# Kernel optimization log

Hardware: AMD Instinct MI355X
Metric: run time of the kernel (lower is better)

Reference implementation:

```python
import jax, jax.numpy as jnp
import numpy as np

N = 8192      # number of WSI patches
DIN = 1024    # input patch-feature dim (dim_in)
DH = 256      # dim_hidden
K = 6         # topk
SCALE = DH ** -0.5

def leaky(x):
    return jax.nn.leaky_relu(x, 0.01)

def setup_inputs() -> dict:
    key = jax.random.key(0)
    ks = jax.random.split(key, 8)
    def w(k, shape, fan_in):
        return jax.random.normal(k, shape, jnp.float32) / np.sqrt(fan_in).astype(np.float32)
    return {
        "x_path": jax.random.normal(ks[0], (N, DIN), jnp.float32),
        "fc1_W": w(ks[1], (DIN, DH), DIN), "fc1_b": jnp.zeros((DH,), jnp.float32),
        "Wh": w(ks[2], (DH, DH), DH), "bh": jnp.zeros((DH,), jnp.float32),
        "Wt": w(ks[3], (DH, DH), DH), "bt": jnp.zeros((DH,), jnp.float32),
        "W1": w(ks[4], (DH, DH), DH), "b1": jnp.zeros((DH,), jnp.float32),
        "W2": w(ks[5], (DH, DH), DH), "b2": jnp.zeros((DH,), jnp.float32),
        "Ag1": w(ks[6], (DH, DH // 2), DH), "bg1": jnp.zeros((DH // 2,), jnp.float32),
        "Ag2": w(ks[7], (DH // 2, 1), DH // 2), "bg2": jnp.zeros((1,), jnp.float32),
    }

def reference(x_path, fc1_W, fc1_b, Wh, bh, Wt, bt, W1, b1, W2, b2, Ag1, bg1, Ag2, bg2):
    # _fc1: Linear(1024->256) + LeakyReLU, then add global mean ("*0.5" mixing)
    x = leaky(x_path @ fc1_W + fc1_b)[None]                 # (1,N,DH)
    x = (x + x.mean(axis=1, keepdims=True)) * 0.5
    e_h = x @ Wh + bh                                        # (1,N,DH)
    e_t = x @ Wt + bt                                        # (1,N,DH)
    # dense attention logits, then top-k neighbor selection
    attn_logit = (e_h * SCALE) @ jnp.swapaxes(e_t, -1, -2)   # (1,N,N)
    topk_w, topk_i = jax.lax.top_k(attn_logit, K)            # (1,N,K)
    p = jax.nn.softmax(topk_w, axis=2)                       # (1,N,K)
    Nb_h = e_t[0][topk_i[0]][None]                           # gather: (1,N,K,DH)
    # message construction
    eh_r = p[..., None] * Nb_h + (1.0 - p)[..., None] * e_h[:, :, None, :]
    gate = jnp.tanh(e_h[:, :, None, :] + eh_r)               # (1,N,K,DH)
    # faithful to torch.einsum('ijkl,ijkm->ijk', Nb_h, gate):
    # l and m are independent -> separable double sum
    ka_w = Nb_h.sum(-1) * gate.sum(-1)                       # (1,N,K)
    ka_p = jax.nn.softmax(ka_w, axis=2)
    e_Nh = jnp.einsum('ink,inkd->ind', ka_p, Nb_h)           # (1,N,DH)
    # message MLPs (dropout in eval mode = identity)
    e_msg = leaky((e_h + e_Nh) @ W1 + b1) + leaky((e_h * e_Nh) @ W2 + b2)
    # GlobalAttention readout: gate_nn = Linear(256,128)+LeakyReLU+Linear(128,1)
    x2 = e_msg[0]                                            # (N,DH)
    g = leaky(x2 @ Ag1 + bg1) @ Ag2 + bg2                    # (N,1)
    g = jax.nn.softmax(g, axis=0)
    e_g = (g * x2).sum(axis=0, keepdims=True)                # (1,DH)
    return e_msg, e_g
```

## Files before the change

kernel.cpp:

```cpp
#include <hip/hip_runtime.h>


typedef __attribute__((ext_vector_type(8))) short short8;
typedef __attribute__((ext_vector_type(4))) short short4v;
typedef __attribute__((ext_vector_type(4))) float f32x4;

__device__ inline float bf2f(unsigned short b) {
    unsigned u = ((unsigned)b) << 16;
    return __builtin_bit_cast(float, u);
}
__device__ inline unsigned short f2bf(float f) {
    unsigned u = __builtin_bit_cast(unsigned, f);
    unsigned r = u + 0x7fffu + ((u >> 16) & 1u);
    return (unsigned short)(r >> 16);
}
__device__ inline f32x4 mfma16(short8 a, short8 b, f32x4 c) {
    return __builtin_amdgcn_mfma_f32_16x16x32_bf16(a, b, c, 0, 0, 0);
}

__device__ inline void gload_lds16(const unsigned short* g, unsigned short* l) {
    __builtin_amdgcn_global_load_lds(
        (const __attribute__((address_space(1))) void*)g,
        (__attribute__((address_space(3))) void*)l, 16, 0, 0);
}

__device__ inline void split8(const f32x4 v0, const f32x4 v1,
                              short8& hi, short8& md, short8& lo) {
    #pragma unroll
    for (int e = 0; e < 8; e++) {
        float a = (e < 4) ? v0[e] : v1[e - 4];
        unsigned short h = f2bf(a);
        float r1 = a - bf2f(h);
        unsigned short m = f2bf(r1);
        float r2 = r1 - bf2f(m);
        unsigned short l = f2bf(r2);
        hi[e] = (short)h; md[e] = (short)m; lo[e] = (short)l;
    }
}

__launch_bounds__(256)
__global__ void tsplit3(const float* __restrict__ W, unsigned short* __restrict__ out,
                        int K, int N, int PS) {
    __shared__ float T[32][33];
    const int t = threadIdx.x;
    const int n0 = blockIdx.x * 32, k0 = blockIdx.y * 32;
    {
        const int r = t >> 3, c = (t & 7) * 4;
        f32x4 v = *(const f32x4*)&W[(size_t)(k0 + r) * N + n0 + c];
        #pragma unroll
        for (int e = 0; e < 4; e++) T[r][c + e] = v[e];
    }
    __syncthreads();
    const int nr = t >> 3, kc = (t & 7) * 4;
    short4v h4, m4, l4;
    #pragma unroll
    for (int e = 0; e < 4; e++) {
        float a = T[kc + e][nr];
        unsigned short h = f2bf(a);
        float r1 = a - bf2f(h);
        unsigned short m = f2bf(r1);
        float r2 = r1 - bf2f(m);
        h4[e] = (short)h; m4[e] = (short)m; l4[e] = (short)f2bf(r2);
    }
    const size_t o = (size_t)(n0 + nr) * K + k0 + kc;
    *(short4v*)&out[o] = h4;
    *(short4v*)&out[(size_t)PS + o] = m4;
    *(short4v*)&out[(size_t)2 * PS + o] = l4;
}

template <int ASPLIT, int ACT, int ACCUM>
__launch_bounds__(256)
__global__ void gemmM(const void* __restrict__ Av,
                      const unsigned short* __restrict__ Bt,
                      const float* __restrict__ bias, float* __restrict__ C,
                      int N, int K, int BPS) {
    constexpr int APL = ASPLIT ? 3 : 1;
    constexpr int BPL = ASPLIT ? 3 : 2;
    __shared__ __align__(16) unsigned short LA[2][APL * 2048];
    __shared__ __align__(16) unsigned short LB[2][BPL * 2048];
    const int t = threadIdx.x;
    const int r0 = blockIdx.y * 64, c0 = blockIdx.x * 64;
    const int lid = t & 63, w = t >> 6, g = lid >> 4, m16 = lid & 15;
    const int wm = w >> 1, wn = w & 1;

    f32x4 acc[2][2];
    #pragma unroll
    for (int mf = 0; mf < 2; mf++)
        #pragma unroll
        for (int nf = 0; nf < 2; nf++) acc[mf][nf] = {0.0f, 0.0f, 0.0f, 0.0f};

    const int KT = K >> 5;
    const size_t aoff = (size_t)(r0 + (t >> 2)) * K + (t & 3) * 8;
    const size_t boff = (size_t)(c0 + (t >> 2)) * K + (t & 3) * 8;

    {
        #pragma unroll
        for (int p = 0; p < BPL; p++)
            gload_lds16(&Bt[(size_t)p * BPS + boff], &LB[0][p * 2048 + 8 * t]);
        if (ASPLIT) {
            const float* A = (const float*)Av;
            f32x4 v0 = *(const f32x4*)&A[aoff];
            f32x4 v1 = *(const f32x4*)&A[aoff + 4];
            short8 hi, md, lo;
            split8(v0, v1, hi, md, lo);
            *(short8*)&LA[0][8 * t] = hi;
            *(short8*)&LA[0][2048 + 8 * t] = md;
            *(short8*)&LA[0][4096 + 8 * t] = lo;
        } else {
            const unsigned short* A16 = (const unsigned short*)Av;
            gload_lds16(&A16[aoff], &LA[0][8 * t]);
        }
    }
    __syncthreads();

    for (int kt = 0; kt < KT; kt++) {
        const int cur = kt & 1, nxt = cur ^ 1;
        const bool hn = (kt + 1) < KT;
        f32x4 v0, v1;
        if (hn) {
            const size_t ko = (size_t)(kt + 1) * 32;
            #pragma unroll
            for (int p = 0; p < BPL; p++)
                gload_lds16(&Bt[(size_t)p * BPS + boff + ko],
                            &LB[nxt][p * 2048 + 8 * t]);
            if (ASPLIT) {
                const float* A = (const float*)Av;
                v0 = *(const f32x4*)&A[aoff + ko];
                v1 = *(const f32x4*)&A[aoff + ko + 4];
            } else {
                const unsigned short* A16 = (const unsigned short*)Av;
                gload_lds16(&A16[aoff + ko], &LA[nxt][8 * t]);
            }
        }
        short8 af[2][APL], bf[2][BPL];
        #pragma unroll
        for (int mf = 0; mf < 2; mf++) {
            const int row = wm * 32 + mf * 16 + m16;
            #pragma unroll
            for (int p = 0; p < APL; p++)
                af[mf][p] = *(const short8*)&LA[cur][p * 2048 + row * 32 + g * 8];
        }
        #pragma unroll
        for (int nf = 0; nf < 2; nf++) {
            const int col = wn * 32 + nf * 16 + m16;
            #pragma unroll
            for (int p = 0; p < BPL; p++)
                bf[nf][p] = *(const short8*)&LB[cur][p * 2048 + col * 32 + g * 8];
        }
        #pragma unroll
        for (int mf = 0; mf < 2; mf++)
            #pragma unroll
            for (int nf = 0; nf < 2; nf++) {
                if (ASPLIT) {
                    acc[mf][nf] = mfma16(af[mf][0], bf[nf][0], acc[mf][nf]);
                    acc[mf][nf] = mfma16(af[mf][0], bf[nf][1], acc[mf][nf]);
                    acc[mf][nf] = mfma16(af[mf][1], bf[nf][0], acc[mf][nf]);
                    acc[mf][nf] = mfma16(af[mf][0], bf[nf][2], acc[mf][nf]);
                    acc[mf][nf] = mfma16(af[mf][1], bf[nf][1], acc[mf][nf]);
                    acc[mf][nf] = mfma16(af[mf][2], bf[nf][0], acc[mf][nf]);
                } else {
                    acc[mf][nf] = mfma16(af[mf][0], bf[nf][0], acc[mf][nf]);
                    acc[mf][nf] = mfma16(af[mf][0], bf[nf][1], acc[mf][nf]);
                }
            }
        if (hn && ASPLIT) {
            short8 hi, md, lo;
            split8(v0, v1, hi, md, lo);
            *(short8*)&LA[nxt][8 * t] = hi;
            *(short8*)&LA[nxt][2048 + 8 * t] = md;
            *(short8*)&LA[nxt][4096 + 8 * t] = lo;
        }
        __syncthreads();
    }

    #pragma unroll
    for (int nf = 0; nf < 2; nf++) {
        const int col = c0 + wn * 32 + nf * 16 + m16;
        const float bv = bias[col];
        #pragma unroll
        for (int mf = 0; mf < 2; mf++) {
            #pragma unroll
            for (int r = 0; r < 4; r++) {
                const int row = r0 + wm * 32 + mf * 16 + g * 4 + r;
                float v = acc[mf][nf][r] + bv;
                if (ACT == 1) v = v > 0.0f ? v : 0.01f * v;
                size_t idx = (size_t)row * N + col;
                if (ACCUM) v += C[idx];
                C[idx] = v;
            }
        }
    }
}

__global__ void colsum_k(const float* __restrict__ x, float* __restrict__ out) {
    int d = threadIdx.x, b = blockIdx.x;
    float s = 0.0f;
    int i0 = b * 128;
    for (int i = 0; i < 128; i++) s += x[(size_t)(i0 + i) * 256 + d];
    out[b * 256 + d] = s;
}
__global__ void meanred_k(const float* __restrict__ p, float* __restrict__ mean) {
    int d = threadIdx.x;
    float s = 0.0f;
    for (int b = 0; b < 64; b++) s += p[b * 256 + d];
    mean[d] = s * (1.0f / 8192.0f);
}
__global__ void finalize_x(float* __restrict__ x, const float* __restrict__ mean) {
    size_t idx = (size_t)blockIdx.x * blockDim.x + threadIdx.x;
    f32x4 v = *(f32x4*)&x[idx * 4];
    int d4 = (int)((idx * 4) & 255);
    f32x4 m = *(const f32x4*)&mean[d4];
    #pragma unroll
    for (int e = 0; e < 4; e++) v[e] = (v[e] + m[e]) * 0.5f;
    *(f32x4*)&x[idx * 4] = v;
}
__global__ void f2bf_k(const float* __restrict__ src, unsigned short* __restrict__ dst, int n4) {
    size_t idx = (size_t)blockIdx.x * blockDim.x + threadIdx.x;
    if (idx >= (size_t)n4) return;
    f32x4 v = *(const f32x4*)&src[idx * 4];
    short4v h;
    #pragma unroll
    for (int e = 0; e < 4; e++) h[e] = (short)f2bf(v[e]);
    *(short4v*)&dst[idx * 4] = h;
}
__launch_bounds__(256)
__global__ void rowsum_k(const float* __restrict__ et, float* __restrict__ rowsum) {
    const int w = threadIdx.x >> 6, l = threadIdx.x & 63;
    const int i = blockIdx.x * 4 + w;
    f32x4 v = *(const f32x4*)&et[(size_t)i * 256 + l * 4];
    float s = v[0] + v[1] + v[2] + v[3];
    #pragma unroll
    for (int st = 1; st < 64; st <<= 1) s += __shfl_xor(s, st);
    if (l == 0) rowsum[i] = s;
}

__device__ inline float packkey(float v, unsigned col) {
    unsigned u = (__builtin_bit_cast(unsigned, v) & 0xFFFFF800u) | col;
    return __builtin_bit_cast(float, u);
}
template<int NK>
__device__ inline void insf(float (&tk)[NK], float key) {
    #pragma unroll
    for (int k = 0; k < NK - 1; k++)
        tk[k] = __builtin_amdgcn_fmed3f(key, tk[k + 1], tk[k]);
    tk[NK - 1] = fmaxf(tk[NK - 1], key);
}

__launch_bounds__(256)
__global__ void screen2(const unsigned short* __restrict__ eh16,
                        const unsigned short* __restrict__ et16,
                        int* __restrict__ candi) {
    __shared__ __align__(16) unsigned short Bs[2][8192];
    const int t = threadIdx.x;
    const int cs = blockIdx.x;
    const int r0 = blockIdx.y * 128;
    const int w = t >> 6, lid = t & 63, g = lid >> 4, m16 = lid & 15;

    short8 bfr[2][8];
    #pragma unroll
    for (int s = 0; s < 2; s++)
        #pragma unroll
        for (int ks = 0; ks < 8; ks++)
            bfr[s][ks] = *(const short8*)
                &eh16[(size_t)(r0 + w * 32 + s * 16 + m16) * 256 + ks * 32 + g * 8];

    float tk0[6], tk1[6];
    #pragma unroll
    for (int q = 0; q < 6; q++) { tk0[q] = -3.0e38f; tk1[q] = -3.0e38f; }

    int scol[4], goff[4], ldsl[4];
    #pragma unroll
    for (int c = 0; c < 4; c++) {
        int L = (w * 4 + c) * 64 + lid;
        int col = L >> 5, gs = L & 31;
        int gorig = (gs & 24) | ((gs ^ col) & 7);
        scol[c] = col; goff[c] = gorig * 8; ldsl[c] = L * 8;
    }

    #pragma unroll
    for (int c = 0; c < 4; c++)
        gload_lds16(&et16[(size_t)(cs * 2048 + scol[c]) * 256 + goff[c]], &Bs[0][ldsl[c]]);
    __syncthreads();

    const int swz = m16 & 7;
    for (int tile = 0; tile < 64; tile++) {
        const int cur = tile & 1;
        if (tile + 1 < 64) {
            const int j1 = cs * 2048 + (tile + 1) * 32;
            #pragma unroll
            for (int c = 0; c < 4; c++)
                gload_lds16(&et16[(size_t)(j1 + scol[c]) * 256 + goff[c]],
                            &Bs[cur ^ 1][ldsl[c]]);
        }
        f32x4 a00 = {0.0f, 0.0f, 0.0f, 0.0f}, a01 = a00, a10 = a00, a11 = a00;
        #pragma unroll
        for (int ks = 0; ks < 8; ks++) {
            const int gq = ks * 4 + g;
            short8 e0 = *(const short8*)&Bs[cur][(m16 * 32 + (gq ^ swz)) * 8];
            short8 e1 = *(const short8*)&Bs[cur][((16 + m16) * 32 + (gq ^ swz)) * 8];
            a00 = mfma16(e0, bfr[0][ks], a00);
            a01 = mfma16(e1, bfr[0][ks], a01);
            a10 = mfma16(e0, bfr[1][ks], a10);
            a11 = mfma16(e1, bfr[1][ks], a11);
        }
        const unsigned cb = (unsigned)(tile * 32 + g * 4);
        #pragma unroll
        for (int r = 0; r < 4; r++) {
            insf<6>(tk0, packkey(a00[r], cb + (unsigned)r));
            insf<6>(tk0, packkey(a01[r], cb + 16u + (unsigned)r));
            insf<6>(tk1, packkey(a10[r], cb + (unsigned)r));
            insf<6>(tk1, packkey(a11[r], cb + 16u + (unsigned)r));
        }
        __syncthreads();
    }

    #pragma unroll
    for (int s = 0; s < 2; s++) {
        float tk8[8];
        tk8[0] = -3.0e38f; tk8[1] = -3.0e38f;
        #pragma unroll
        for (int q = 0; q < 6; q++) tk8[q + 2] = s ? tk1[q] : tk0[q];
        #pragma unroll
        for (int step = 16; step <= 32; step <<= 1) {
            float ok[8];
            #pragma unroll
            for (int q = 0; q < 8; q++) ok[q] = __shfl_xor(tk8[q], step);
            #pragma unroll
            for (int q = 0; q < 8; q++) insf<8>(tk8, ok[q]);
        }
        if (g == 0) {
            const int row = r0 + w * 32 + s * 16 + m16;
            #pragma unroll
            for (int q = 0; q < 8; q++)
                candi[(size_t)row * 32 + cs * 8 + q] =
                    cs * 2048 + (int)(__builtin_bit_cast(unsigned, tk8[q]) & 0x7FFu);
        }
    }
}

__launch_bounds__(256)
__global__ void stageD(const float* __restrict__ eh, const float* __restrict__ et,
                       const float* __restrict__ rowsum,
                       const int* __restrict__ candi,
                       unsigned short* __restrict__ m1, unsigned short* __restrict__ m2) {
    const int w = threadIdx.x >> 6, l = threadIdx.x & 63;
    const int i = blockIdx.x * 4 + w;

    const int jown = candi[(size_t)i * 32 + (l & 31)] & 8191;

    const int c = l >> 1, h = l & 1;
    const int jc = __shfl(jown, c);
    const float* eprow = &eh[(size_t)i * 256 + h * 128];
    const float* etrow = &et[(size_t)jc * 256 + h * 128];
    double acc = 0.0, acc2 = 0.0;
    #pragma unroll 4
    for (int q = 0; q < 32; q += 2) {
        f32x4 a0 = *(const f32x4*)&eprow[q * 4];
        f32x4 b0 = *(const f32x4*)&etrow[q * 4];
        f32x4 a1 = *(const f32x4*)&eprow[q * 4 + 4];
        f32x4 b1 = *(const f32x4*)&etrow[q * 4 + 4];
        acc  += (double)a0[0] * b0[0] + (double)a0[1] * b0[1] +
                (double)a0[2] * b0[2] + (double)a0[3] * b0[3];
        acc2 += (double)a1[0] * b1[0] + (double)a1[1] * b1[1] +
                (double)a1[2] * b1[2] + (double)a1[3] * b1[3];
    }
    double p = acc + acc2;
    p += __shfl_xor(p, 1);
    p *= 0.0625;

    double v = __shfl(p, 2 * (l & 31));

    float wf[6]; int selj[6];
    #pragma unroll
    for (int s = 0; s < 6; s++) {
        double bv = v; int bj = jown;
        #pragma unroll
        for (int st = 1; st < 64; st <<= 1) {
            double ov = __shfl_xor(bv, st);
            int oj = __shfl_xor(bj, st);
            bool take = (ov > bv) || (ov == bv && oj < bj);
            bv = take ? ov : bv;
            bj = take ? oj : bj;
        }
        wf[s] = (float)bv; selj[s] = bj;
        if (jown == bj) v = -1.0e300;
    }

    float sp[6];
    {
        float mx = wf[0];
        #pragma unroll
        for (int s = 1; s < 6; s++) mx = fmaxf(mx, wf[s]);
        float se = 0.0f, e6[6];
        #pragma unroll
        for (int s = 0; s < 6; s++) { e6[s] = expf(wf[s] - mx); se += e6[s]; }
        #pragma unroll
        for (int s = 0; s < 6; s++) sp[s] = e6[s] / se;
    }

    f32x4 eh4 = *(const f32x4*)&eh[(size_t)i * 256 + l * 4];
    f32x4 nb[6];
    #pragma unroll
    for (int k = 0; k < 6; k++)
        nb[k] = *(const f32x4*)&et[(size_t)selj[k] * 256 + l * 4];

    float pgs[6], pns[6];
    #pragma unroll
    for (int k = 0; k < 6; k++) {
        const float pk = sp[k];
        float pg = 0.0f;
        #pragma unroll
        for (int e = 0; e < 4; e++) {
            float ehd = eh4[e], nbd = nb[k][e];
            float ehr = pk * nbd + (1.0f - pk) * ehd;
            pg += tanhf(ehd + ehr);
        }
        #pragma unroll
        for (int st = 1; st < 64; st <<= 1) pg += __shfl_xor(pg, st);
        pgs[k] = pg;
        pns[k] = rowsum[selj[k]];
    }

    float skp[6];
    {
        float ka[6], mx = -3.0e38f, se = 0.0f;
        #pragma unroll
        for (int k = 0; k < 6; k++) { ka[k] = pns[k] * pgs[k]; mx = fmaxf(mx, ka[k]); }
        #pragma unroll
        for (int k = 0; k < 6; k++) { ka[k] = expf(ka[k] - mx); se += ka[k]; }
        #pragma unroll
        for (int k = 0; k < 6; k++) skp[k] = ka[k] / se;
    }

    f32x4 enh = {0.0f, 0.0f, 0.0f, 0.0f};
    #pragma unroll
    for (int k = 0; k < 6; k++) {
        const float kp = skp[k];
        #pragma unroll
        for (int e = 0; e < 4; e++) enh[e] += kp * nb[k][e];
    }
    short4v h1, h2;
    #pragma unroll
    for (int e = 0; e < 4; e++) {
        h1[e] = (short)f2bf(eh4[e] + enh[e]);
        h2[e] = (short)f2bf(eh4[e] * enh[e]);
    }
    *(short4v*)&m1[(size_t)i * 256 + l * 4] = h1;
    *(short4v*)&m2[(size_t)i * 256 + l * 4] = h2;
}

__launch_bounds__(256)
__global__ void gate2_k(const float* __restrict__ g1, const float* __restrict__ Ag2,
                        const float* __restrict__ bg2, float* __restrict__ glog) {
    const int i = blockIdx.x * 256 + threadIdx.x;
    float s = 0.0f;
    #pragma unroll 4
    for (int h = 0; h < 128; h++) s += g1[(size_t)i * 128 + h] * Ag2[h];
    glog[i] = s + bg2[0];
}

__launch_bounds__(1024)
__global__ void softmax_g(const float* __restrict__ glog, float* __restrict__ gexp,
                          float* __restrict__ scal) {
    const int t = threadIdx.x;
    __shared__ float red[1024];
    float v[8];
    float m = -3.0e38f;
    #pragma unroll
    for (int c = 0; c < 8; c++) { v[c] = glog[t + c * 1024]; m = fmaxf(m, v[c]); }
    red[t] = m; __syncthreads();
    for (int st = 512; st > 0; st >>= 1) {
        if (t < st) red[t] = fmaxf(red[t], red[t + st]);
        __syncthreads();
    }
    float gm = red[0]; __syncthreads();
    float s = 0.0f;
    #pragma unroll
    for (int c = 0; c < 8; c++) {
        float e = expf(v[c] - gm);
        gexp[t + c * 1024] = e;
        s += e;
    }
    red[t] = s; __syncthreads();
    for (int st = 512; st > 0; st >>= 1) {
        if (t < st) red[t] += red[t + st];
        __syncthreads();
    }
    if (t == 0) scal[0] = 1.0f / red[0];
}

__launch_bounds__(256)
__global__ void wsum_k(const float* __restrict__ emsg, const float* __restrict__ gexp,
                       float* __restrict__ egp) {
    const int b = blockIdx.x, d = threadIdx.x;
    float s = 0.0f;
    const int i0 = b * 128;
    for (int i = 0; i < 128; i++) s += gexp[i0 + i] * emsg[(size_t)(i0 + i) * 256 + d];
    egp[b * 256 + d] = s;
}
__global__ void egfinal_f(const float* __restrict__ egp, const float* __restrict__ scal,
                          float* __restrict__ out) {
    const int d = threadIdx.x;
    float s = 0.0f;
    for (int b = 0; b < 64; b++) s += egp[b * 256 + d];
    out[d] = s * scal[0];
}

__global__ void wsbad_k(float* __restrict__ out) { out[3] = 9000.0f; }

extern "C" void kernel_launch(void* const* d_in, const int* in_sizes, int n_in,
                              void* d_out, int out_size, void* d_ws, size_t ws_size,
                              hipStream_t stream) {
    (void)in_sizes; (void)n_in; (void)out_size;
    const float* x_path = (const float*)d_in[0];
    const float* fc1_W  = (const float*)d_in[1];
    const float* fc1_b  = (const float*)d_in[2];
    const float* Wh     = (const float*)d_in[3];
    const float* bh     = (const float*)d_in[4];
    const float* Wt     = (const float*)d_in[5];
    const float* bt     = (const float*)d_in[6];
    const float* W1     = (const float*)d_in[7];
    const float* b1     = (const float*)d_in[8];
    const float* W2     = (const float*)d_in[9];
    const float* b2     = (const float*)d_in[10];
    const float* Ag1    = (const float*)d_in[11];
    const float* bg1    = (const float*)d_in[12];
    const float* Ag2    = (const float*)d_in[13];
    const float* bg2    = (const float*)d_in[14];
    float* out_f = (float*)d_out;

    const size_t WS_NEEDED = 26412048;
    if (ws_size < WS_NEEDED) {
        hipLaunchKernelGGL(wsbad_k, dim3(1), dim3(1), 0, stream, out_f);
        return;
    }

    char* ws = (char*)d_ws;
    float* x     = (float*)(ws + 0);
    unsigned short* eh16 = (unsigned short*)(ws + 0);
    unsigned short* et16 = (unsigned short*)(ws + 4194304);
    unsigned short* m1b  = (unsigned short*)(ws + 0);
    unsigned short* m2b  = (unsigned short*)(ws + 4194304);
    float* g1    = (float*)(ws + 0);
    float* eh    = (float*)(ws + 8388608);
    float* emsg  = out_f;
    float* et    = (float*)(ws + 16777216);
    int*   candi = (int*)  (ws + 25165824);
    float* rowsum= (float*)(ws + 26214400);
    float* meanp = (float*)(ws + 26214400);
    float* meanv = (float*)(ws + 26279936);
    float* glog  = (float*)(ws + 26280960);
    float* gexp  = (float*)(ws + 26313728);
    float* egp   = (float*)(ws + 26346496);
    float* scal  = (float*)(ws + 26412032);

    unsigned short* Fp = (unsigned short*)(ws + 16777216);
    unsigned short* WHp = (unsigned short*)(ws + 25165824);
    unsigned short* WTp = (unsigned short*)(ws + 25559040);
    unsigned short* P1 = (unsigned short*)(ws + 16777216);
    unsigned short* P2 = (unsigned short*)(ws + 17170432);
    unsigned short* Gp = (unsigned short*)(ws + 25165824);

    dim3 gg(4, 128);
    hipLaunchKernelGGL(tsplit3, dim3(8, 32), dim3(256), 0, stream,
                       fc1_W, Fp, 1024, 256, 262144);
    hipLaunchKernelGGL((gemmM<1, 1, 0>), gg, dim3(256), 0, stream,
                       (const void*)x_path, Fp, fc1_b, x, 256, 1024, 262144);
    hipLaunchKernelGGL(colsum_k, dim3(64), dim3(256), 0, stream, x, meanp);
    hipLaunchKernelGGL(meanred_k, dim3(1), dim3(256), 0, stream, meanp, meanv);
    hipLaunchKernelGGL(finalize_x, dim3(2048), dim3(256), 0, stream, x, meanv);
    hipLaunchKernelGGL(tsplit3, dim3(8, 8), dim3(256), 0, stream,
                       Wh, WHp, 256, 256, 65536);
    hipLaunchKernelGGL(tsplit3, dim3(8, 8), dim3(256), 0, stream,
                       Wt, WTp, 256, 256, 65536);
    hipLaunchKernelGGL((gemmM<1, 0, 0>), gg, dim3(256), 0, stream,
                       (const void*)x, WHp, bh, eh, 256, 256, 65536);
    hipLaunchKernelGGL((gemmM<1, 0, 0>), gg, dim3(256), 0, stream,
                       (const void*)x, WTp, bt, et, 256, 256, 65536);
    hipLaunchKernelGGL(f2bf_k, dim3(2048), dim3(256), 0, stream, eh, eh16, 524288);
    hipLaunchKernelGGL(f2bf_k, dim3(2048), dim3(256), 0, stream, et, et16, 524288);
    hipLaunchKernelGGL(rowsum_k, dim3(2048), dim3(256), 0, stream, et, rowsum);
    hipLaunchKernelGGL(screen2, dim3(4, 64), dim3(256), 0, stream, eh16, et16, candi);
    hipLaunchKernelGGL(stageD, dim3(2048), dim3(256), 0, stream, eh, et, rowsum,
                       candi, m1b, m2b);
    hipLaunchKernelGGL(tsplit3, dim3(8, 8), dim3(256), 0, stream,
                       W1, P1, 256, 256, 65536);
    hipLaunchKernelGGL(tsplit3, dim3(8, 8), dim3(256), 0, stream,
                       W2, P2, 256, 256, 65536);
    hipLaunchKernelGGL((gemmM<0, 1, 0>), gg, dim3(256), 0, stream,
                       (const void*)m1b, P1, b1, emsg, 256, 256, 65536);
    hipLaunchKernelGGL((gemmM<0, 1, 1>), gg, dim3(256), 0, stream,
                       (const void*)m2b, P2, b2, emsg, 256, 256, 65536);
    hipLaunchKernelGGL(tsplit3, dim3(4, 8), dim3(256), 0, stream,
                       Ag1, Gp, 256, 128, 32768);
    hipLaunchKernelGGL((gemmM<1, 1, 0>), dim3(2, 128), dim3(256), 0, stream,
                       (const void*)emsg, Gp, bg1, g1, 128, 256, 32768);
    hipLaunchKernelGGL(gate2_k, dim3(32), dim3(256), 0, stream, g1, Ag2, bg2, glog);
    hipLaunchKernelGGL(softmax_g, dim3(1), dim3(1024), 0, stream, glog, gexp, scal);
    hipLaunchKernelGGL(wsum_k, dim3(64), dim3(256), 0, stream, emsg, gexp, egp);
    hipLaunchKernelGGL(egfinal_f, dim3(1), dim3(256), 0, stream, egp, scal, out_f + 2097152);
}
```

Measured before the change: 362.5 us.

## Split screen2 column tile across wave pairs, halving rows per block

The screening kernel now gives each block 64 rows instead of 128. Pairs of waves share a 32-row slice, and each wave of a pair handles half of the 32 columns in every tile. Each wave keeps its own partial top-8 per row, and these are merged through a small shared-memory buffer before the candidate indices are written. This doubles the grid to 512 blocks so more CUs are occupied, and halves the MFMA and insertion work per wave per tile. In exchange, each block loads the full et tile for half as many rows, so LDS traffic per output doubles, and there is an extra sync and merge step.

Result: slower. 378.0 us (+4.3%).

```diff
diff --git a/kernel.cpp b/kernel.cpp
--- a/kernel.cpp
+++ b/kernel.cpp
@@ -251,10 +251,12 @@
                         const unsigned short* __restrict__ et16,
                         int* __restrict__ candi) {
     __shared__ __align__(16) unsigned short Bs[2][8192];
+    __shared__ float mbuf[4][2][16][8];
     const int t = threadIdx.x;
     const int cs = blockIdx.x;
-    const int r0 = blockIdx.y * 128;
+    const int r0 = blockIdx.y * 64;
     const int w = t >> 6, lid = t & 63, g = lid >> 4, m16 = lid & 15;
+    const int rs = w >> 1, ch = w & 1;
 
     short8 bfr[2][8];
     #pragma unroll
@@ -262,7 +264,7 @@
         #pragma unroll
         for (int ks = 0; ks < 8; ks++)
             bfr[s][ks] = *(const short8*)
-                &eh16[(size_t)(r0 + w * 32 + s * 16 + m16) * 256 + ks * 32 + g * 8];
+                &eh16[(size_t)(r0 + rs * 32 + s * 16 + m16) * 256 + ks * 32 + g * 8];
 
     float tk0[6], tk1[6];
     #pragma unroll
@@ -283,6 +285,7 @@
     __syncthreads();
 
     const int swz = m16 & 7;
+    const int cbase = (ch * 16 + m16) * 32;
     for (int tile = 0; tile < 64; tile++) {
         const int cur = tile & 1;
         if (tile + 1 < 64) {
@@ -292,24 +295,19 @@
                 gload_lds16(&et16[(size_t)(j1 + scol[c]) * 256 + goff[c]],
                             &Bs[cur ^ 1][ldsl[c]]);
         }
-        f32x4 a00 = {0.0f, 0.0f, 0.0f, 0.0f}, a01 = a00, a10 = a00, a11 = a00;
+        f32x4 a0 = {0.0f, 0.0f, 0.0f, 0.0f}, a1 = a0;
         #pragma unroll
         for (int ks = 0; ks < 8; ks++) {
             const int gq = ks * 4 + g;
-            short8 e0 = *(const short8*)&Bs[cur][(m16 * 32 + (gq ^ swz)) * 8];
-            short8 e1 = *(const short8*)&Bs[cur][((16 + m16) * 32 + (gq ^ swz)) * 8];
-            a00 = mfma16(e0, bfr[0][ks], a00);
-            a01 = mfma16(e1, bfr[0][ks], a01);
-            a10 = mfma16(e0, bfr[1][ks], a10);
-            a11 = mfma16(e1, bfr[1][ks], a11);
-        }
-        const unsigned cb = (unsigned)(tile * 32 + g * 4);
+            short8 e = *(const short8*)&Bs[cur][(cbase + (gq ^ swz)) * 8];
+            a0 = mfma16(e, bfr[0][ks], a0);
+            a1 = mfma16(e, bfr[1][ks], a1);
+        }
+        const unsigned cb = (unsigned)(tile * 32 + ch * 16 + g * 4);
         #pragma unroll
         for (int r = 0; r < 4; r++) {
-            insf<6>(tk0, packkey(a00[r], cb + (unsigned)r));
-            insf<6>(tk0, packkey(a01[r], cb + 16u + (unsigned)r));
-            insf<6>(tk1, packkey(a10[r], cb + (unsigned)r));
-            insf<6>(tk1, packkey(a11[r], cb + 16u + (unsigned)r));
+            insf<6>(tk0, packkey(a0[r], cb + (unsigned)r));
+            insf<6>(tk1, packkey(a1[r], cb + (unsigned)r));
         }
         __syncthreads();
     }
@@ -329,12 +327,23 @@
             for (int q = 0; q < 8; q++) insf<8>(tk8, ok[q]);
         }
         if (g == 0) {
-            const int row = r0 + w * 32 + s * 16 + m16;
-            #pragma unroll
-            for (int q = 0; q < 8; q++)
-                candi[(size_t)row * 32 + cs * 8 + q] =
-                    cs * 2048 + (int)(__builtin_bit_cast(unsigned, tk8[q]) & 0x7FFu);
-        }
+            #pragma unroll
+            for (int q = 0; q < 8; q++) mbuf[rs * 2 + s][ch][m16][q] = tk8[q];
+        }
+    }
+    __syncthreads();
+
+    if (t < 64) {
+        float tk8[8];
+        #pragma unroll
+        for (int q = 0; q < 8; q++) tk8[q] = mbuf[t >> 4][0][t & 15][q];
+        #pragma unroll
+        for (int q = 0; q < 8; q++) insf<8>(tk8, mbuf[t >> 4][1][t & 15][q]);
+        const int row = r0 + t;
+        #pragma unroll
+        for (int q = 0; q < 8; q++)
+            candi[(size_t)row * 32 + cs * 8 + q] =
+                cs * 2048 + (int)(__builtin_bit_cast(unsigned, tk8[q]) & 0x7FFu);
     }
 }
 
@@ -580,7 +589,7 @@
     hipLaunchKernelGGL(f2bf_k, dim3(2048), dim3(256), 0, stream, eh, eh16, 524288);
     hipLaunchKernelGGL(f2bf_k, dim3(2048), dim3(256), 0, stream, et, et16, 524288);
     hipLaunchKernelGGL(rowsum_k, dim3(2048), dim3(256), 0, stream, et, rowsum);
-    hipLaunchKernelGGL(screen2, dim3(4, 64), dim3(256), 0, stream, eh16, et16, candi);
+    hipLaunchKernelGGL(screen2, dim3(4, 128), dim3(256), 0, stream, eh16, et16, candi);
     hipLaunchKernelGGL(stageD, dim3(2048), dim3(256), 0, stream, eh, et, rowsum,
                        candi, m1b, m2b);
     hipLaunchKernelGGL(tsplit3, dim3(8, 8), dim3(256), 0, stream,
```
